# Kernel tuning notes

Hardware: AMD Instinct MI355X
Metric: run time of the kernel (lower is better)

## Reference

```python
import jax, jax.numpy as jnp
import numpy as np

EPS = 1e-5  # torch GroupNorm default


def setup_inputs() -> dict:
    key = jax.random.key(0)
    ks = jax.random.split(key, 7)
    B, H, W, C = 8, 64, 64, 64
    x = jax.random.normal(ks[0], (B, H, W, C), dtype=jnp.float32)
    temb = jax.random.normal(ks[1], (B, 256), dtype=jnp.float32)
    scale = 0.02
    Wq = jax.random.normal(ks[2], (C, C), dtype=jnp.float32) * scale
    Wk = jax.random.normal(ks[3], (C, C), dtype=jnp.float32) * scale
    Wv = jax.random.normal(ks[4], (C, C), dtype=jnp.float32) * scale
    Wo = jax.random.normal(ks[5], (C, C), dtype=jnp.float32) * scale
    z = jnp.zeros((C,), dtype=jnp.float32)
    return {"x": x, "temb": temb, "Wq": Wq, "bq": z, "Wk": Wk, "bk": z,
            "Wv": Wv, "bv": z, "Wo": Wo, "bo": z}


def reference(x, temb, Wq, bq, Wk, bk, Wv, bv, Wo, bo):
    # x: [B, H, W, C] channels-last. temb is accepted but unused (as in source).
    B, H, W, C = x.shape
    S = H * W
    # normalize(): freshly-built GroupNorm(num_groups=1) with identity affine
    # -> standardize over all non-batch dims.
    mu = jnp.mean(x, axis=(1, 2, 3), keepdims=True)
    var = jnp.var(x, axis=(1, 2, 3), keepdims=True)
    h = (x - mu) * jax.lax.rsqrt(var + EPS)
    hf = h.reshape(B, S, C)
    q = hf @ Wq.T + bq  # [B, S, C]
    k = hf @ Wk.T + bk
    v = hf @ Wv.T + bv
    # full (S x S) score matrix, scaled by C^-0.5, naive softmax
    w = jnp.einsum('bsc,btc->bst', q, k) * (C ** -0.5)
    w = jax.nn.softmax(w, axis=-1)
    o = jnp.einsum('bst,btc->bsc', w, v)  # [B, S, C]
    o = o @ Wo.T + bo
    return x + o.reshape(B, H, W, C)
```

## Files before the change

kernel.cpp:

```cpp
#include <hip/hip_runtime.h>
#include <hip/hip_bf16.h>
#include <math.h>

#define B_ 8
#define S_ 4096
#define C_ 64
#define EPSV 1e-5f

using floatx4 = __attribute__((ext_vector_type(4))) float;
using bf16x8  = __attribute__((ext_vector_type(8))) short;
using bf16x4  = __attribute__((ext_vector_type(4))) short;

typedef __attribute__((address_space(3))) unsigned int       as3_u32;
typedef __attribute__((address_space(1))) const unsigned int as1_u32;

__device__ __forceinline__ short f2bf(float f) {
    unsigned u = __builtin_bit_cast(unsigned, f);
    u = u + 0x7fffu + ((u >> 16) & 1u);
    return (short)(u >> 16);
}

__device__ __forceinline__ float bf2f(short s) {
    return __builtin_bit_cast(float, ((unsigned)(unsigned short)s) << 16);
}

__device__ __forceinline__ unsigned cvt_pk_bf16(float lo, float hi) {
    unsigned r;
    asm volatile("v_cvt_pk_bf16_f32 %0, %1, %2" : "=v"(r) : "v"(lo), "v"(hi));
    return r;
}

__device__ __forceinline__ floatx4 mfma_16x16x16_bf16(bf16x4 a, bf16x4 b, floatx4 c) {
#if __has_builtin(__builtin_amdgcn_mfma_f32_16x16x16bf16_1k)
    return __builtin_amdgcn_mfma_f32_16x16x16bf16_1k(a, b, c, 0, 0, 0);
#else
    asm("v_mfma_f32_16x16x16_bf16 %0, %1, %2, %0" : "+v"(c) : "v"(a), "v"(b));
    return c;
#endif
}

__device__ __forceinline__ bf16x8 ld_w_frag(const float* __restrict__ W, int n, int kk, int g, int c) {
    const float* p = W + (16 * n + c) * C_ + 32 * kk + 8 * g;
    bf16x8 r;
#pragma unroll
    for (int j = 0; j < 8; ++j) r[j] = f2bf(p[j]);
    return r;
}

__global__ __launch_bounds__(256) void stats1_kernel(const float* __restrict__ x,
                                                     float* __restrict__ partial) {
    int b = blockIdx.x >> 5, chunk = blockIdx.x & 31;
    const float4* xb = (const float4*)x + (size_t)b * 65536 + chunk * 2048;
    float s = 0.f, ss = 0.f;
#pragma unroll
    for (int i = 0; i < 8; ++i) {
        float4 v = xb[threadIdx.x + i * 256];
        s  += v.x + v.y + v.z + v.w;
        ss += v.x * v.x + v.y * v.y + v.z * v.z + v.w * v.w;
    }
    for (int off = 32; off > 0; off >>= 1) {
        s  += __shfl_down(s, off);
        ss += __shfl_down(ss, off);
    }
    __shared__ float sm[4], ssm[4];
    int wid = threadIdx.x >> 6, lane = threadIdx.x & 63;
    if (lane == 0) { sm[wid] = s; ssm[wid] = ss; }
    __syncthreads();
    if (threadIdx.x == 0) {
        partial[blockIdx.x * 2]     = sm[0] + sm[1] + sm[2] + sm[3];
        partial[blockIdx.x * 2 + 1] = ssm[0] + ssm[1] + ssm[2] + ssm[3];
    }
}

__global__ __launch_bounds__(512) void stats2_kernel(const float* __restrict__ partial,
                                                     float* __restrict__ stats) {
    int w = threadIdx.x >> 6, lane = threadIdx.x & 63;
    float s = 0.f, ss = 0.f;
    if (lane < 32) {
        s  = partial[(w * 32 + lane) * 2];
        ss = partial[(w * 32 + lane) * 2 + 1];
    }
    for (int off = 16; off > 0; off >>= 1) {
        s  += __shfl_down(s, off);
        ss += __shfl_down(ss, off);
    }
    if (lane == 0) {
        const float invN = 1.0f / (float)(S_ * C_);
        float mu  = s * invN;
        float var = ss * invN - mu * mu;
        stats[w * 2]     = mu;
        stats[w * 2 + 1] = rsqrtf(var + EPSV);
    }
}

__global__ __launch_bounds__(256) void proj_kernel(
    const float* __restrict__ x,
    const float* __restrict__ Wq, const float* __restrict__ bq,
    const float* __restrict__ Wk, const float* __restrict__ bk,
    const float* __restrict__ Wv, const float* __restrict__ bv,
    const float* __restrict__ stats,
    short* __restrict__ qo, char* __restrict__ kws, char* __restrict__ vws) {
    __shared__ char hbuf[64 * 128];

    int b  = blockIdx.x >> 6;
    int t_ = blockIdx.x & 63;
    int s0 = t_ * 64;
    float mu = stats[b * 2], rs = stats[b * 2 + 1];
    const float* xt = x + ((size_t)b * S_ + s0) * C_;
    int t = threadIdx.x;

#pragma unroll
    for (int i = 0; i < 4; ++i) {
        int fi  = t + 256 * i;
        int row = fi >> 4;
        int c4  = fi & 15;
        float4 v = *(const float4*)(xt + row * C_ + c4 * 4);
        unsigned lo = (unsigned)(unsigned short)f2bf((v.x - mu) * rs) |
                      ((unsigned)(unsigned short)f2bf((v.y - mu) * rs) << 16);
        unsigned hi = (unsigned)(unsigned short)f2bf((v.z - mu) * rs) |
                      ((unsigned)(unsigned short)f2bf((v.w - mu) * rs) << 16);
        int off = row * 128 + c4 * 8;
        off ^= (row & 7) << 4;
        *(uint2*)(hbuf + off) = make_uint2(lo, hi);
    }
    __syncthreads();

    int lane = t & 63, w = t >> 6;
    int g = lane >> 4, c = lane & 15;

    auto ld_h = [&](int row, int kcol) -> bf16x8 {
        int off = row * 128 + kcol * 2;
        off ^= (row & 7) << 4;
        return *(const bf16x8*)(hbuf + off);
    };

    size_t tilebase = ((size_t)b * 64 + t_) * 8192;

    bf16x8 ha[2];
    ha[0] = ld_h(16 * w + c, 8 * g);
    ha[1] = ld_h(16 * w + c, 32 + 8 * g);

    const float QSC = 0.125f * 1.44269504088896340736f;

#pragma unroll
    for (int n = 0; n < 4; ++n) {
        floatx4 aq = {0.f, 0.f, 0.f, 0.f}, ak = {0.f, 0.f, 0.f, 0.f};
#pragma unroll
        for (int kk = 0; kk < 2; ++kk) {
            bf16x8 wq = ld_w_frag(Wq, n, kk, g, c);
            bf16x8 wk = ld_w_frag(Wk, n, kk, g, c);
            aq = __builtin_amdgcn_mfma_f32_16x16x32_bf16(ha[kk], wq, aq, 0, 0, 0);
            ak = __builtin_amdgcn_mfma_f32_16x16x32_bf16(ha[kk], wk, ak, 0, 0, 0);
        }
        float bqv = bq[16 * n + c], bkv = bk[16 * n + c];
#pragma unroll
        for (int r = 0; r < 4; ++r) {
            int rr = 16 * w + 4 * g + r;
            qo[((size_t)b * S_ + s0 + rr) * C_ + 16 * n + c] = f2bf((aq[r] + bqv) * QSC);
            int koff = (rr * 128 + (16 * n + c) * 2) ^ ((rr & 7) << 4);
            *(short*)(kws + tilebase + koff) = f2bf(ak[r] + bkv);
        }
    }

    bf16x8 wv[2];
    wv[0] = ld_w_frag(Wv, w, 0, g, c);
    wv[1] = ld_w_frag(Wv, w, 1, g, c);
    float bvr[4];
#pragma unroll
    for (int r = 0; r < 4; ++r) bvr[r] = bv[16 * w + 4 * g + r];

#pragma unroll
    for (int n = 0; n < 4; ++n) {
        floatx4 av = {0.f, 0.f, 0.f, 0.f};
#pragma unroll
        for (int kk = 0; kk < 2; ++kk) {
            bf16x8 hb = ld_h(16 * n + c, 32 * kk + 8 * g);
            av = __builtin_amdgcn_mfma_f32_16x16x32_bf16(wv[kk], hb, av, 0, 0, 0);
        }
#pragma unroll
        for (int r = 0; r < 4; ++r) {
            int rr = 16 * w + 4 * g + r;
            int u  = 16 * n + c;
            int voff = (rr * 128 + u * 2) ^ ((rr & 7) << 4);
            *(short*)(vws + tilebase + voff) = f2bf(av[r] + bvr[r]);
        }
    }
}

__global__ __launch_bounds__(256) void flash_kernel(
    const short* __restrict__ qm, const char* __restrict__ kws, const char* __restrict__ vws,
    short* __restrict__ Opart, float2* __restrict__ mlpart) {
    __shared__ char lds[32768];

    int bid = blockIdx.x;
    int logical = (bid & 7) * 128 + (bid >> 3);
    int b = logical >> 7;
    int rest = logical & 127;
    int q0 = (rest >> 1) * 64;
    int half = rest & 1;
    int t = threadIdx.x;
    int lane = t & 63, w = t >> 6;
    int g = lane >> 4, c = lane & 15;
    int qw = q0 + 16 * w;

    const char* kbase = kws + (size_t)b * 64 * 8192;
    const char* vbase = vws + (size_t)b * 64 * 8192;
    const short* qp = qm + (size_t)b * S_ * C_;

    bf16x8 bqf[2];
    bqf[0] = *(const bf16x8*)(qp + (qw + c) * C_ + 8 * g);
    bqf[1] = *(const bf16x8*)(qp + (qw + c) * C_ + 32 + 8 * g);

    floatx4 oacc[4];
#pragma unroll
    for (int n = 0; n < 4; ++n) oacc[n] = (floatx4){0.f, 0.f, 0.f, 0.f};
    float m = -__builtin_inff(), lsum = 0.f;

    const int xmask = (c & 7) << 4;

    auto STAGE = [&](int bi, int tt) {
        const char* gk = kbase + (size_t)tt * 8192 + w * 2048 + lane * 16;
        const char* gv = vbase + (size_t)tt * 8192 + w * 2048 + lane * 16;
        char* lk = lds +         bi * 8192 + w * 2048 + lane * 16;
        char* lv = lds + 16384 + bi * 8192 + w * 2048 + lane * 16;
        __builtin_amdgcn_global_load_lds((as1_u32*)gk,          (as3_u32*)lk,          16, 0, 0);
        __builtin_amdgcn_global_load_lds((as1_u32*)(gk + 1024), (as3_u32*)(lk + 1024), 16, 0, 0);
        __builtin_amdgcn_global_load_lds((as1_u32*)gv,          (as3_u32*)lv,          16, 0, 0);
        __builtin_amdgcn_global_load_lds((as1_u32*)(gv + 1024), (as3_u32*)(lv + 1024), 16, 0, 0);
    };

    auto ld_k = [&](const char* buf, int subtile, int colb) -> bf16x8 {
        return *(const bf16x8*)(buf + subtile * 2048 + c * 128 + (colb ^ xmask));
    };
    auto ld_v = [&](const char* buf, int mi, int s) -> bf16x4 {
        return *(const bf16x4*)(buf + mi * 2048 + c * 128 + ((32 * s + 8 * g) ^ xmask));
    };

    auto COMPUTE = [&](int bi) {
        const char* kbuf = lds +         bi * 8192;
        const char* vbuf = lds + 16384 + bi * 8192;
        floatx4 st[4];
        __builtin_amdgcn_s_setprio(1);
#pragma unroll
        for (int s = 0; s < 4; ++s) {
            st[s] = (floatx4){0.f, 0.f, 0.f, 0.f};
#pragma unroll
            for (int kk = 0; kk < 2; ++kk) {
                bf16x8 ak = ld_k(kbuf, s, 64 * kk + 16 * g);
                st[s] = __builtin_amdgcn_mfma_f32_16x16x32_bf16(ak, bqf[kk], st[s], 0, 0, 0);
            }
        }
        __builtin_amdgcn_s_setprio(0);
        float mt = st[0][0];
#pragma unroll
        for (int s = 0; s < 4; ++s)
#pragma unroll
            for (int r = 0; r < 4; ++r) mt = fmaxf(mt, st[s][r]);
        mt = fmaxf(mt, __shfl_xor(mt, 16));
        mt = fmaxf(mt, __shfl_xor(mt, 32));
        if (!__all(mt - m <= 8.0f)) {
            float mnew  = fmaxf(m, mt);
            float alpha = __builtin_amdgcn_exp2f(m - mnew);
            lsum *= alpha;
            m = mnew;
#pragma unroll
            for (int n = 0; n < 4; ++n) oacc[n] *= alpha;
        }
        bf16x4 pb[4];
        float psum = 0.f;
#pragma unroll
        for (int s = 0; s < 4; ++s) {
            float e0 = __builtin_amdgcn_exp2f(st[s][0] - m);
            float e1 = __builtin_amdgcn_exp2f(st[s][1] - m);
            float e2 = __builtin_amdgcn_exp2f(st[s][2] - m);
            float e3 = __builtin_amdgcn_exp2f(st[s][3] - m);
            psum += (e0 + e1) + (e2 + e3);
            uint2 u = make_uint2(cvt_pk_bf16(e0, e1), cvt_pk_bf16(e2, e3));
            pb[s] = __builtin_bit_cast(bf16x4, u);
        }
        lsum += psum;
        __builtin_amdgcn_s_setprio(1);
#pragma unroll
        for (int s = 0; s < 4; ++s) {
#pragma unroll
            for (int mi = 0; mi < 4; ++mi) {
                bf16x4 av = ld_v(vbuf, mi, s);
                oacc[mi] = mfma_16x16x16_bf16(av, pb[s], oacc[mi]);
            }
        }
        __builtin_amdgcn_s_setprio(0);
    };

    const int base = half * 32;
    STAGE(0, base);
    __syncthreads();
    for (int r = 0; r < 32; r += 2) {
        STAGE(1, base + r + 1);
        COMPUTE(0);
        __syncthreads();
        if (r + 2 < 32) STAGE(0, base + r + 2);
        COMPUTE(1);
        __syncthreads();
    }

    lsum += __shfl_xor(lsum, 16);
    lsum += __shfl_xor(lsum, 32);

    size_t prow = (size_t)(half * 8 + b) * S_ + q0;
    if (lane < 16)
        mlpart[prow + 16 * w + lane] = make_float2(m, lsum);

    short* op = Opart + (prow + 16 * w + c) * C_;
#pragma unroll
    for (int mi = 0; mi < 4; ++mi) {
        uint2 u = make_uint2(cvt_pk_bf16(oacc[mi][0], oacc[mi][1]),
                             cvt_pk_bf16(oacc[mi][2], oacc[mi][3]));
        *(uint2*)(op + 16 * mi + 4 * g) = u;
    }
}

__global__ __launch_bounds__(256) void combine_kernel(
    const short* __restrict__ Opart, const float2* __restrict__ mlpart,
    const float* __restrict__ Wo, const float* __restrict__ bo,
    const float* __restrict__ x, float* __restrict__ out) {
    __shared__ char obuf[8192];

    int bid = blockIdx.x;
    int logical = (bid & 7) * 64 + (bid >> 3);
    int b = logical >> 6;
    int q0 = (logical & 63) * 64;
    int t = threadIdx.x;
    int lane = t & 63, w = t >> 6;
    int g = lane >> 4, c = lane & 15;

    const short*  P0  = Opart  + ((size_t)b * S_ + q0) * C_;
    const short*  P1  = Opart  + ((size_t)(8 + b) * S_ + q0) * C_;
    const float2* ml0 = mlpart + (size_t)b * S_ + q0;
    const float2* ml1 = mlpart + (size_t)(8 + b) * S_ + q0;

#pragma unroll
    for (int i = 0; i < 16; ++i) {
        int idx = t + 256 * i;
        int q = idx >> 6, ch = idx & 63;
        float2 a0 = ml0[q], a1 = ml1[q];
        float M  = fmaxf(a0.x, a1.x);
        float s0 = __builtin_amdgcn_exp2f(a0.x - M);
        float s1 = __builtin_amdgcn_exp2f(a1.x - M);
        float L  = a0.y * s0 + a1.y * s1;
        float o  = (bf2f(P0[q * 64 + ch]) * s0 + bf2f(P1[q * 64 + ch]) * s1) / L;
        int off = (q * 128 + ch * 2) ^ ((q & 7) << 4);
        *(short*)(obuf + off) = f2bf(o);
    }
    __syncthreads();

    bf16x8 ao[2];
    {
        int row = 16 * w + c;
        int off0 = (row * 128 + (8 * g) * 2)      ^ ((row & 7) << 4);
        int off1 = (row * 128 + (32 + 8 * g) * 2) ^ ((row & 7) << 4);
        ao[0] = *(const bf16x8*)(obuf + off0);
        ao[1] = *(const bf16x8*)(obuf + off1);
    }
#pragma unroll
    for (int n = 0; n < 4; ++n) {
        floatx4 a = {0.f, 0.f, 0.f, 0.f};
#pragma unroll
        for (int kk = 0; kk < 2; ++kk) {
            bf16x8 bw = ld_w_frag(Wo, n, kk, g, c);
            a = __builtin_amdgcn_mfma_f32_16x16x32_bf16(ao[kk], bw, a, 0, 0, 0);
        }
        float bov = bo[16 * n + c];
#pragma unroll
        for (int r = 0; r < 4; ++r) {
            int srow = q0 + 16 * w + 4 * g + r;
            size_t idx = ((size_t)b * S_ + srow) * C_ + 16 * n + c;
            out[idx] = x[idx] + bov + a[r];
        }
    }
}

extern "C" void kernel_launch(void* const* d_in, const int* in_sizes, int n_in,
                              void* d_out, int out_size, void* d_ws, size_t ws_size,
                              hipStream_t stream) {
    const float* x  = (const float*)d_in[0];
    const float* Wq = (const float*)d_in[2];
    const float* bq = (const float*)d_in[3];
    const float* Wk = (const float*)d_in[4];
    const float* bk = (const float*)d_in[5];
    const float* Wv = (const float*)d_in[6];
    const float* bv = (const float*)d_in[7];
    const float* Wo = (const float*)d_in[8];
    const float* bo = (const float*)d_in[9];
    float* out = (float*)d_out;

    char* ws = (char*)d_ws;
    float*  partial = (float*)ws;
    float*  stats   = (float*)(ws + 2048);
    short*  q   = (short*)(ws + 4096);
    char*   kt  = (char*)(q + (size_t)B_ * S_ * C_);
    char*   vt  = kt + (size_t)B_ * 64 * 8192;
    short*  op  = (short*)(vt + (size_t)B_ * 64 * 8192);
    float2* mlp = (float2*)((char*)op + (size_t)2 * B_ * S_ * C_ * 2);

    stats1_kernel<<<256, 256, 0, stream>>>(x, partial);
    stats2_kernel<<<1, 512, 0, stream>>>(partial, stats);
    proj_kernel<<<B_ * (S_ / 64), 256, 0, stream>>>(x, Wq, bq, Wk, bk, Wv, bv, stats, q, kt, vt);
    flash_kernel<<<B_ * (S_ / 64) * 2, 256, 0, stream>>>(q, kt, vt, op, mlp);
    combine_kernel<<<B_ * (S_ / 64), 256, 0, stream>>>(op, mlp, Wo, bo, x, out);
}
```

Measured before the change: 91.55 us.

## Split KV range into four parts with 32-row tiles and smaller LDS

```diff
diff --git a/kernel.cpp b/kernel.cpp
--- a/kernel.cpp
+++ b/kernel.cpp
@@ -134,8 +134,6 @@
         return *(const bf16x8*)(hbuf + off);
     };
 
-    size_t tilebase = ((size_t)b * 64 + t_) * 8192;
-
     bf16x8 ha[2];
     ha[0] = ld_h(16 * w + c, 8 * g);
     ha[1] = ld_h(16 * w + c, 32 + 8 * g);
@@ -157,8 +155,10 @@
         for (int r = 0; r < 4; ++r) {
             int rr = 16 * w + 4 * g + r;
             qo[((size_t)b * S_ + s0 + rr) * C_ + 16 * n + c] = f2bf((aq[r] + bqv) * QSC);
-            int koff = (rr * 128 + (16 * n + c) * 2) ^ ((rr & 7) << 4);
-            *(short*)(kws + tilebase + koff) = f2bf(ak[r] + bkv);
+            int r32 = rr & 31;
+            size_t tb = ((size_t)b * 128 + 2 * t_ + (rr >> 5)) * 4096;
+            int koff = (r32 * 128 + (16 * n + c) * 2) ^ ((r32 & 7) << 4);
+            *(short*)(kws + tb + koff) = f2bf(ak[r] + bkv);
         }
     }
 
@@ -177,34 +177,36 @@
             bf16x8 hb = ld_h(16 * n + c, 32 * kk + 8 * g);
             av = __builtin_amdgcn_mfma_f32_16x16x32_bf16(wv[kk], hb, av, 0, 0, 0);
         }
+        int u   = 16 * n + c;
+        int u32 = u & 31;
+        size_t tb = ((size_t)b * 128 + 2 * t_ + (u >> 5)) * 4096;
 #pragma unroll
         for (int r = 0; r < 4; ++r) {
             int rr = 16 * w + 4 * g + r;
-            int u  = 16 * n + c;
-            int voff = (rr * 128 + u * 2) ^ ((rr & 7) << 4);
-            *(short*)(vws + tilebase + voff) = f2bf(av[r] + bvr[r]);
-        }
-    }
-}
-
-__global__ __launch_bounds__(256) void flash_kernel(
+            int voff = (rr * 64 + u32 * 2) ^ ((rr & 7) << 3);
+            *(short*)(vws + tb + voff) = f2bf(av[r] + bvr[r]);
+        }
+    }
+}
+
+__global__ __launch_bounds__(256, 8) void flash_kernel(
     const short* __restrict__ qm, const char* __restrict__ kws, const char* __restrict__ vws,
     short* __restrict__ Opart, float2* __restrict__ mlpart) {
-    __shared__ char lds[32768];
+    __shared__ char lds[16384];
 
     int bid = blockIdx.x;
-    int logical = (bid & 7) * 128 + (bid >> 3);
-    int b = logical >> 7;
-    int rest = logical & 127;
-    int q0 = (rest >> 1) * 64;
-    int half = rest & 1;
+    int logical = (bid & 7) * 256 + (bid >> 3);
+    int b = logical >> 8;
+    int rest = logical & 255;
+    int q0 = (rest >> 2) * 64;
+    int quarter = rest & 3;
     int t = threadIdx.x;
     int lane = t & 63, w = t >> 6;
     int g = lane >> 4, c = lane & 15;
     int qw = q0 + 16 * w;
 
-    const char* kbase = kws + (size_t)b * 64 * 8192;
-    const char* vbase = vws + (size_t)b * 64 * 8192;
+    const char* kbase = kws + (size_t)b * 128 * 4096;
+    const char* vbase = vws + (size_t)b * 128 * 4096;
     const short* qp = qm + (size_t)b * S_ * C_;
 
     bf16x8 bqf[2];
@@ -216,33 +218,32 @@
     for (int n = 0; n < 4; ++n) oacc[n] = (floatx4){0.f, 0.f, 0.f, 0.f};
     float m = -__builtin_inff(), lsum = 0.f;
 
-    const int xmask = (c & 7) << 4;
+    const int xmask  = (c & 7) << 4;
+    const int vxmask = (c & 7) << 3;
 
     auto STAGE = [&](int bi, int tt) {
-        const char* gk = kbase + (size_t)tt * 8192 + w * 2048 + lane * 16;
-        const char* gv = vbase + (size_t)tt * 8192 + w * 2048 + lane * 16;
-        char* lk = lds +         bi * 8192 + w * 2048 + lane * 16;
-        char* lv = lds + 16384 + bi * 8192 + w * 2048 + lane * 16;
-        __builtin_amdgcn_global_load_lds((as1_u32*)gk,          (as3_u32*)lk,          16, 0, 0);
-        __builtin_amdgcn_global_load_lds((as1_u32*)(gk + 1024), (as3_u32*)(lk + 1024), 16, 0, 0);
-        __builtin_amdgcn_global_load_lds((as1_u32*)gv,          (as3_u32*)lv,          16, 0, 0);
-        __builtin_amdgcn_global_load_lds((as1_u32*)(gv + 1024), (as3_u32*)(lv + 1024), 16, 0, 0);
+        const char* gk = kbase + (size_t)tt * 4096 + t * 16;
+        const char* gv = vbase + (size_t)tt * 4096 + t * 16;
+        char* lk = lds +        bi * 4096 + t * 16;
+        char* lv = lds + 8192 + bi * 4096 + t * 16;
+        __builtin_amdgcn_global_load_lds((as1_u32*)gk, (as3_u32*)lk, 16, 0, 0);
+        __builtin_amdgcn_global_load_lds((as1_u32*)gv, (as3_u32*)lv, 16, 0, 0);
     };
 
-    auto ld_k = [&](const char* buf, int subtile, int colb) -> bf16x8 {
-        return *(const bf16x8*)(buf + subtile * 2048 + c * 128 + (colb ^ xmask));
+    auto ld_k = [&](const char* buf, int s, int colb) -> bf16x8 {
+        return *(const bf16x8*)(buf + s * 2048 + c * 128 + (colb ^ xmask));
     };
     auto ld_v = [&](const char* buf, int mi, int s) -> bf16x4 {
-        return *(const bf16x4*)(buf + mi * 2048 + c * 128 + ((32 * s + 8 * g) ^ xmask));
+        return *(const bf16x4*)(buf + mi * 1024 + c * 64 + ((32 * s + 8 * g) ^ vxmask));
     };
 
     auto COMPUTE = [&](int bi) {
-        const char* kbuf = lds +         bi * 8192;
-        const char* vbuf = lds + 16384 + bi * 8192;
-        floatx4 st[4];
+        const char* kbuf = lds +        bi * 4096;
+        const char* vbuf = lds + 8192 + bi * 4096;
+        floatx4 st[2];
         __builtin_amdgcn_s_setprio(1);
 #pragma unroll
-        for (int s = 0; s < 4; ++s) {
+        for (int s = 0; s < 2; ++s) {
             st[s] = (floatx4){0.f, 0.f, 0.f, 0.f};
 #pragma unroll
             for (int kk = 0; kk < 2; ++kk) {
@@ -253,7 +254,7 @@
         __builtin_amdgcn_s_setprio(0);
         float mt = st[0][0];
 #pragma unroll
-        for (int s = 0; s < 4; ++s)
+        for (int s = 0; s < 2; ++s)
 #pragma unroll
             for (int r = 0; r < 4; ++r) mt = fmaxf(mt, st[s][r]);
         mt = fmaxf(mt, __shfl_xor(mt, 16));
@@ -266,10 +267,10 @@
 #pragma unroll
             for (int n = 0; n < 4; ++n) oacc[n] *= alpha;
         }
-        bf16x4 pb[4];
+        bf16x4 pb[2];
         float psum = 0.f;
 #pragma unroll
-        for (int s = 0; s < 4; ++s) {
+        for (int s = 0; s < 2; ++s) {
             float e0 = __builtin_amdgcn_exp2f(st[s][0] - m);
             float e1 = __builtin_amdgcn_exp2f(st[s][1] - m);
             float e2 = __builtin_amdgcn_exp2f(st[s][2] - m);
@@ -281,7 +282,7 @@
         lsum += psum;
         __builtin_amdgcn_s_setprio(1);
 #pragma unroll
-        for (int s = 0; s < 4; ++s) {
+        for (int s = 0; s < 2; ++s) {
 #pragma unroll
             for (int mi = 0; mi < 4; ++mi) {
                 bf16x4 av = ld_v(vbuf, mi, s);
@@ -291,7 +292,7 @@
         __builtin_amdgcn_s_setprio(0);
     };
 
-    const int base = half * 32;
+    const int base = quarter * 32;
     STAGE(0, base);
     __syncthreads();
     for (int r = 0; r < 32; r += 2) {
@@ -306,7 +307,7 @@
     lsum += __shfl_xor(lsum, 16);
     lsum += __shfl_xor(lsum, 32);
 
-    size_t prow = (size_t)(half * 8 + b) * S_ + q0;
+    size_t prow = (size_t)(quarter * 8 + b) * S_ + q0;
     if (lane < 16)
         mlpart[prow + 16 * w + lane] = make_float2(m, lsum);
 
@@ -333,21 +334,27 @@
     int lane = t & 63, w = t >> 6;
     int g = lane >> 4, c = lane & 15;
 
-    const short*  P0  = Opart  + ((size_t)b * S_ + q0) * C_;
-    const short*  P1  = Opart  + ((size_t)(8 + b) * S_ + q0) * C_;
-    const float2* ml0 = mlpart + (size_t)b * S_ + q0;
-    const float2* ml1 = mlpart + (size_t)(8 + b) * S_ + q0;
+    const short*  P[4];
+    const float2* ml[4];
+#pragma unroll
+    for (int h = 0; h < 4; ++h) {
+        P[h]  = Opart  + ((size_t)(h * 8 + b) * S_ + q0) * C_;
+        ml[h] = mlpart + (size_t)(h * 8 + b) * S_ + q0;
+    }
 
 #pragma unroll
     for (int i = 0; i < 16; ++i) {
         int idx = t + 256 * i;
         int q = idx >> 6, ch = idx & 63;
-        float2 a0 = ml0[q], a1 = ml1[q];
-        float M  = fmaxf(a0.x, a1.x);
+        float2 a0 = ml[0][q], a1 = ml[1][q], a2 = ml[2][q], a3 = ml[3][q];
+        float M = fmaxf(fmaxf(a0.x, a1.x), fmaxf(a2.x, a3.x));
         float s0 = __builtin_amdgcn_exp2f(a0.x - M);
         float s1 = __builtin_amdgcn_exp2f(a1.x - M);
-        float L  = a0.y * s0 + a1.y * s1;
-        float o  = (bf2f(P0[q * 64 + ch]) * s0 + bf2f(P1[q * 64 + ch]) * s1) / L;
+        float s2 = __builtin_amdgcn_exp2f(a2.x - M);
+        float s3 = __builtin_amdgcn_exp2f(a3.x - M);
+        float L  = a0.y * s0 + a1.y * s1 + a2.y * s2 + a3.y * s3;
+        float o  = (bf2f(P[0][q * 64 + ch]) * s0 + bf2f(P[1][q * 64 + ch]) * s1 +
+                    bf2f(P[2][q * 64 + ch]) * s2 + bf2f(P[3][q * 64 + ch]) * s3) / L;
         int off = (q * 128 + ch * 2) ^ ((q & 7) << 4);
         *(short*)(obuf + off) = f2bf(o);
     }
@@ -398,13 +405,13 @@
     float*  stats   = (float*)(ws + 2048);
     short*  q   = (short*)(ws + 4096);
     char*   kt  = (char*)(q + (size_t)B_ * S_ * C_);
-    char*   vt  = kt + (size_t)B_ * 64 * 8192;
-    short*  op  = (short*)(vt + (size_t)B_ * 64 * 8192);
-    float2* mlp = (float2*)((char*)op + (size_t)2 * B_ * S_ * C_ * 2);
+    char*   vt  = kt + (size_t)B_ * 128 * 4096;
+    short*  op  = (short*)(vt + (size_t)B_ * 128 * 4096);
+    float2* mlp = (float2*)((char*)op + (size_t)4 * B_ * S_ * C_ * 2);
 
     stats1_kernel<<<256, 256, 0, stream>>>(x, partial);
     stats2_kernel<<<1, 512, 0, stream>>>(partial, stats);
     proj_kernel<<<B_ * (S_ / 64), 256, 0, stream>>>(x, Wq, bq, Wk, bk, Wv, bv, stats, q, kt, vt);
-    flash_kernel<<<B_ * (S_ / 64) * 2, 256, 0, stream>>>(q, kt, vt, op, mlp);
+    flash_kernel<<<B_ * (S_ / 64) * 4, 256, 0, stream>>>(q, kt, vt, op, mlp);
     combine_kernel<<<B_ * (S_ / 64), 256, 0, stream>>>(op, mlp, Wo, bo, x, out);
 }
```

Result: slower. 93.74 us (+2.4%).
